# Kernel optimization log

Hardware: AMD Instinct MI355X
Metric: run time of the kernel (lower is better)

The kernel has to match this reference:

```python
import jax, jax.numpy as jnp
import numpy as np

N = 20000
D = 256      # input_dim
F = 256      # output_dim
K = F // 8   # hypernetwork rank (c=8 in source)


def setup_inputs() -> dict:
    key = jax.random.key(0)
    k1, k2, k3, k4, k5 = jax.random.split(key, 5)
    h = jax.random.normal(k1, (N, D), dtype=jnp.float32)
    adj = jax.random.uniform(k2, (N, N), dtype=jnp.float32)
    # xavier-uniform-like small init for params
    W1 = jax.random.normal(k3, (D, K), dtype=jnp.float32) * 0.05
    W2 = jax.random.normal(k4, (K, D, F), dtype=jnp.float32) * 0.05
    b = jax.random.normal(k5, (K, F), dtype=jnp.float32) * 0.05
    return {"h": h, "adj": adj, "W1": W1, "W2": W2, "b": b}


def reference(h, adj, W1, W2, b):
    # node: per-node code vector [N, K]
    node = h @ W1
    # Original: w = einsum('nd,dcf->ncf', node, W2); x = einsum('nc,ncf->nf', h, w)
    # Algebraically identical but avoids the huge [N, D, F] intermediate by
    # contracting the input-dim axis first: [N,K,F] instead of [N,D,F].
    hw = jnp.einsum('nc,kcf->nkf', h, W2)      # [N, K, F]
    x = jnp.einsum('nk,nkf->nf', node, hw)     # [N, F]
    # graph aggregation
    x = adj @ x                                 # [N, F]
    # per-node bias generated from the node code
    x = x + node @ b                            # [N, F]
    return jax.nn.relu(x)
```

## Files before the change

kernel.cpp:

```cpp
#include <hip/hip_runtime.h>
#include <hip/hip_bf16.h>

#define Nn 20000
#define Dd 256
#define Ff 256
#define Kc 32

typedef __attribute__((ext_vector_type(8))) short short8;
typedef __attribute__((ext_vector_type(4))) short short4_t;
typedef __attribute__((ext_vector_type(4))) float float4_t;

static __device__ __forceinline__ short f2bf(float x) {
    union { float f; unsigned u; } v; v.f = x;
    unsigned r = v.u + 0x7FFFu + ((v.u >> 16) & 1u);
    return (short)(r >> 16);
}
static __device__ __forceinline__ short4_t cvt4(float4_t v) {
    short4_t r; r[0] = f2bf(v[0]); r[1] = f2bf(v[1]); r[2] = f2bf(v[2]); r[3] = f2bf(v[3]);
    return r;
}

__global__ __launch_bounds__(256) void k_node(const float* __restrict__ h,
                                              const float* __restrict__ W1,
                                              float* __restrict__ node) {
    int t = blockIdx.x * 256 + threadIdx.x;
    int n = t >> 5, k = t & 31;
    if (n >= Nn) return;
    const float4_t* hr = (const float4_t*)(h + (size_t)n * Dd);
    float s = 0.f;
    #pragma unroll 8
    for (int d4 = 0; d4 < 64; ++d4) {
        float4_t hv = hr[d4];
        #pragma unroll
        for (int j = 0; j < 4; ++j) s += hv[j] * W1[(d4 * 4 + j) * Kc + k];
    }
    node[n * Kc + k] = s;
}

__global__ __launch_bounds__(256) void k_packW2(const float* __restrict__ W2,
                                                short* __restrict__ P) {
    int t = blockIdx.x * 256 + threadIdx.x;
    int lane = t & 63;
    int cf = (t >> 6) & 15;
    int dc = (t >> 10) & 7;
    int kk = t >> 13;
    int col = cf * 16 + (lane & 15);
    int d0  = dc * 32 + (lane >> 4) * 8;
    const float* src = W2 + ((size_t)(kk * Dd + d0)) * Ff + col;
    short8 v;
    #pragma unroll
    for (int j = 0; j < 8; ++j) v[j] = f2bf(src[(size_t)j * Ff]);
    *(short8*)(P + (size_t)t * 8) = v;
}

__global__ __launch_bounds__(256, 2) void k_xpre(const float* __restrict__ h,
                                                 const float* __restrict__ node,
                                                 const short* __restrict__ P,
                                                 short* __restrict__ xpre_t) {
    __shared__ short hlds[64 * 264];
    __shared__ float ntl[32 * 64];
    int t = threadIdx.x;
    int n0 = blockIdx.x * 64;

    #pragma unroll
    for (int i = 0; i < 16; ++i) {
        int c = t + i * 256;
        int row = c >> 6, cc = c & 63;
        int n = n0 + row; if (n > Nn - 1) n = Nn - 1;
        float4_t v = *(const float4_t*)(h + (size_t)n * Dd + cc * 4);
        *(short4_t*)&hlds[row * 264 + cc * 4] = cvt4(v);
    }
    #pragma unroll
    for (int i = 0; i < 8; ++i) {
        int idx = t + i * 256;
        int nl = idx >> 5, k = idx & 31;
        int n = n0 + nl; if (n > Nn - 1) n = Nn - 1;
        ntl[k * 64 + nl] = node[(size_t)n * Kc + k];
    }
    __syncthreads();

    int lane = t & 63, w = t >> 6;
    int arow = lane & 15;
    int asel = (lane >> 4) * 8;
    float4_t acc[4][4];
    #pragma unroll
    for (int a = 0; a < 4; ++a)
        #pragma unroll
        for (int b2 = 0; b2 < 4; ++b2) acc[a][b2] = (float4_t){0.f, 0.f, 0.f, 0.f};

    for (int kk = 0; kk < 32; ++kk) {
        float4_t T[4][4];
        #pragma unroll
        for (int a = 0; a < 4; ++a)
            #pragma unroll
            for (int b2 = 0; b2 < 4; ++b2) T[a][b2] = (float4_t){0.f, 0.f, 0.f, 0.f};
        #pragma unroll
        for (int dc = 0; dc < 8; ++dc) {
            short8 af[4], bfr[4];
            #pragma unroll
            for (int rf = 0; rf < 4; ++rf)
                af[rf] = *(const short8*)&hlds[(rf * 16 + arow) * 264 + dc * 32 + asel];
            #pragma unroll
            for (int cf = 0; cf < 4; ++cf)
                bfr[cf] = *(const short8*)(P + ((size_t)(((kk * 8 + dc) * 16 + w * 4 + cf) * 64 + lane)) * 8);
            #pragma unroll
            for (int rf = 0; rf < 4; ++rf)
                #pragma unroll
                for (int cf = 0; cf < 4; ++cf)
                    T[rf][cf] = __builtin_amdgcn_mfma_f32_16x16x32_bf16(af[rf], bfr[cf], T[rf][cf], 0, 0, 0);
        }
        #pragma unroll
        for (int rf = 0; rf < 4; ++rf) {
            float4_t sc = *(const float4_t*)&ntl[kk * 64 + rf * 16 + (lane >> 4) * 4];
            #pragma unroll
            for (int cf = 0; cf < 4; ++cf)
                #pragma unroll
                for (int r = 0; r < 4; ++r)
                    acc[rf][cf][r] += sc[r] * T[rf][cf][r];
        }
    }

    #pragma unroll
    for (int rf = 0; rf < 4; ++rf) {
        int nl = rf * 16 + (lane >> 4) * 4;
        #pragma unroll
        for (int cf = 0; cf < 4; ++cf) {
            int f = w * 64 + cf * 16 + (lane & 15);
            #pragma unroll
            for (int r = 0; r < 4; ++r) {
                int n = n0 + nl + r;
                if (n < Nn) xpre_t[(size_t)f * Nn + n] = f2bf(acc[rf][cf][r]);
            }
        }
    }
}

#define BM 80
#define BK 160
#define ASTR 168
#define NSTEP 125

__global__ __launch_bounds__(512, 2) void k_aggr(const float* __restrict__ adj,
                                                 const short* __restrict__ xpre_t,
                                                 const float* __restrict__ node,
                                                 const float* __restrict__ bb,
                                                 float* __restrict__ out) {
    __shared__ short alds[2][BM * ASTR];
    __shared__ float nlds[BM * 32];
    __shared__ float blds[32 * 256];

    const int t = threadIdx.x;
    const int m0 = blockIdx.x * BM;
    const int lane = t & 63, w = t >> 6;
    const int kb = (lane >> 4) * 8;

    #pragma unroll
    for (int i = 0; i < 5; ++i) { int idx = t + i * 512; nlds[idx] = node[(size_t)m0 * 32 + idx]; }
    #pragma unroll
    for (int i = 0; i < 4; ++i) { int idx = t + i * 512; *(float4_t*)&blds[idx * 4] = *(const float4_t*)(bb + (size_t)idx * 4); }

    const bool val7 = (t < 128);
    long gbase[7]; int loff[7];
    #pragma unroll
    for (int i = 0; i < 7; ++i) {
        int c = t + i * 512; if (c >= 3200) c = 0;
        int row = c / 40, col = c % 40;
        gbase[i] = (long)(m0 + row) * Nn + col * 4;
        loff[i]  = row * ASTR + col * 4;
    }
    const long xb0 = (long)(w * 32 + (lane & 15)) * Nn + kb;
    const long xb1 = xb0 + 16L * Nn;

#define LOADA(dst, s_) do { _Pragma("unroll") for (int i = 0; i < 7; ++i) \
        if (i < 6 || val7) dst[i] = *(const float4_t*)(adj + gbase[i] + (long)(s_) * BK); } while (0)

#define WRITEA(src, buf_) do { _Pragma("unroll") for (int i = 0; i < 7; ++i) \
        if (i < 6 || val7) *(short4_t*)&alds[buf_][loff[i]] = cvt4(src[i]); } while (0)

#define LOADB(d0_, d1_, s_) do { _Pragma("unroll") for (int dc = 0; dc < 5; ++dc) { \
        d0_[dc] = *(const short8*)(xpre_t + xb0 + (long)(s_) * BK + dc * 32); \
        d1_[dc] = *(const short8*)(xpre_t + xb1 + (long)(s_) * BK + dc * 32); } } while (0)

#define COMPUTE(buf_, B0_, B1_) do { _Pragma("unroll") for (int dc = 0; dc < 5; ++dc) { \
        _Pragma("unroll") for (int rf = 0; rf < 5; ++rf) { \
            short8 afr = *(const short8*)&alds[buf_][(rf * 16 + (lane & 15)) * ASTR + dc * 32 + kb]; \
            acc[rf][0] = __builtin_amdgcn_mfma_f32_16x16x32_bf16(afr, B0_[dc], acc[rf][0], 0, 0, 0); \
            acc[rf][1] = __builtin_amdgcn_mfma_f32_16x16x32_bf16(afr, B1_[dc], acc[rf][1], 0, 0, 0); } } } while (0)

#define SYNC() do { asm volatile("s_waitcnt lgkmcnt(0)" ::: "memory"); \
                    __builtin_amdgcn_s_barrier(); } while (0)

    float4_t acc[5][2];
    #pragma unroll
    for (int rf = 0; rf < 5; ++rf)
        #pragma unroll
        for (int cf = 0; cf < 2; ++cf) acc[rf][cf] = (float4_t){0.f, 0.f, 0.f, 0.f};

    float4_t A0[7], A1[7];
    short8 BA0[5], BA1[5], BB0[5], BB1[5];

    LOADA(A0, 0);
    LOADA(A1, 1);
    LOADB(BA0, BA1, 0);
    LOADB(BB0, BB1, 1);
    WRITEA(A0, 0);
    SYNC();

    #pragma unroll 1
    for (int p = 0; p < 62; ++p) {
        const int s0 = 2 * p;
        LOADA(A0, s0 + 2);
        COMPUTE(0, BA0, BA1);
        LOADB(BA0, BA1, s0 + 2);
        WRITEA(A1, 1);
        SYNC();
        if (s0 + 3 < NSTEP) LOADA(A1, s0 + 3);
        COMPUTE(1, BB0, BB1);
        if (s0 + 3 < NSTEP) LOADB(BB0, BB1, s0 + 3);
        WRITEA(A0, 0);
        SYNC();
    }
    COMPUTE(0, BA0, BA1);

    #pragma unroll
    for (int rf = 0; rf < 5; ++rf) {
        #pragma unroll
        for (int cf = 0; cf < 2; ++cf) {
            int fl = w * 32 + cf * 16 + (lane & 15);
            #pragma unroll
            for (int r = 0; r < 4; ++r) {
                int nl = rf * 16 + (lane >> 4) * 4 + r;
                float bias = 0.f;
                #pragma unroll 8
                for (int k = 0; k < 32; ++k) bias += nlds[nl * 32 + k] * blds[k * 256 + fl];
                float v = acc[rf][cf][r] + bias;
                out[(size_t)(m0 + nl) * 256 + fl] = v > 0.f ? v : 0.f;
            }
        }
    }
#undef LOADA
#undef WRITEA
#undef LOADB
#undef COMPUTE
#undef SYNC
}

extern "C" void kernel_launch(void* const* d_in, const int* in_sizes, int n_in,
                              void* d_out, int out_size, void* d_ws, size_t ws_size,
                              hipStream_t stream) {
    const float* h   = (const float*)d_in[0];
    const float* adj = (const float*)d_in[1];
    const float* W1  = (const float*)d_in[2];
    const float* W2  = (const float*)d_in[3];
    const float* b   = (const float*)d_in[4];
    float* out = (float*)d_out;

    char* ws = (char*)d_ws;
    float* node   = (float*)ws;
    short* P      = (short*)(ws + 2560000);
    short* xpre_t = (short*)(ws + 2560000 + 4194304);

    k_node  <<<2500, 256, 0, stream>>>(h, W1, node);
    k_packW2<<<1024, 256, 0, stream>>>(W2, P);
    k_xpre  <<<313,  256, 0, stream>>>(h, node, P, xpre_t);
    k_aggr  <<<250,  512, 0, stream>>>(adj, xpre_t, node, b, out);
}
```

Measured before the change: 868.3 us.

## Double BK to 320, pad xpre_t, restructure aggregation pipeline single-stage

Doubles the K-tile of the adj@x aggregation to 320 columns, which gives 63 steps with one barrier each. The single-step pipeline prefetches the next adj tile into registers while the MFMAs run, replacing the earlier two-stage register double-buffering. xpre_t is padded to 20160 columns and zero-filled so the last partial tile reads zeros, and adj reads are clamped to stay in bounds. The fp32 to bf16 conversion now uses the packed v_cvt_pk_bf16_f32 instruction. The changes aim to cut barrier and loop overhead, but they use more LDS and registers per block, which may lower occupancy under the 2-blocks-per-SM launch bound.

```diff
diff --git a/kernel.cpp b/kernel.cpp
--- a/kernel.cpp
+++ b/kernel.cpp
@@ -2,6 +2,7 @@
 #include <hip/hip_bf16.h>
 
 #define Nn 20000
+#define Npad 20160
 #define Dd 256
 #define Ff 256
 #define Kc 32
@@ -9,6 +10,7 @@
 typedef __attribute__((ext_vector_type(8))) short short8;
 typedef __attribute__((ext_vector_type(4))) short short4_t;
 typedef __attribute__((ext_vector_type(4))) float float4_t;
+typedef __attribute__((ext_vector_type(2))) unsigned int uint2_t;
 
 static __device__ __forceinline__ short f2bf(float x) {
     union { float f; unsigned u; } v; v.f = x;
@@ -17,6 +19,11 @@
 }
 static __device__ __forceinline__ short4_t cvt4(float4_t v) {
     short4_t r; r[0] = f2bf(v[0]); r[1] = f2bf(v[1]); r[2] = f2bf(v[2]); r[3] = f2bf(v[3]);
+    return r;
+}
+static __device__ __forceinline__ unsigned cvtpk(float a, float b) {
+    unsigned r;
+    asm("v_cvt_pk_bf16_f32 %0, %1, %2" : "=v"(r) : "v"(a), "v"(b));
     return r;
 }
 
@@ -129,16 +136,19 @@
             #pragma unroll
             for (int r = 0; r < 4; ++r) {
                 int n = n0 + nl + r;
-                if (n < Nn) xpre_t[(size_t)f * Nn + n] = f2bf(acc[rf][cf][r]);
+                if (n < Nn)       xpre_t[(size_t)f * Npad + n] = f2bf(acc[rf][cf][r]);
+                else if (n < Npad) xpre_t[(size_t)f * Npad + n] = 0;
             }
         }
     }
 }
 
 #define BM 80
-#define BK 160
-#define ASTR 168
-#define NSTEP 125
+#define BK 320
+#define DCN 10
+#define ASTR 328
+#define NSTEP 63
+#define ALIM (Nn * Nn - 4)
 
 __global__ __launch_bounds__(512, 2) void k_aggr(const float* __restrict__ adj,
                                                  const short* __restrict__ xpre_t,
@@ -159,68 +169,68 @@
     #pragma unroll
     for (int i = 0; i < 4; ++i) { int idx = t + i * 512; *(float4_t*)&blds[idx * 4] = *(const float4_t*)(bb + (size_t)idx * 4); }
 
-    const bool val7 = (t < 128);
-    long gbase[7]; int loff[7];
-    #pragma unroll
-    for (int i = 0; i < 7; ++i) {
-        int c = t + i * 512; if (c >= 3200) c = 0;
-        int row = c / 40, col = c % 40;
-        gbase[i] = (long)(m0 + row) * Nn + col * 4;
+    const bool v13 = (t < 256);
+    int gbase[13], loff[13];
+    #pragma unroll
+    for (int i = 0; i < 13; ++i) {
+        int c = t + i * 512; if (c >= 6400) c = 0;
+        int row = c / 80, col = c % 80;
+        gbase[i] = (m0 + row) * Nn + col * 4;
         loff[i]  = row * ASTR + col * 4;
     }
-    const long xb0 = (long)(w * 32 + (lane & 15)) * Nn + kb;
-    const long xb1 = xb0 + 16L * Nn;
-
-#define LOADA(dst, s_) do { _Pragma("unroll") for (int i = 0; i < 7; ++i) \
-        if (i < 6 || val7) dst[i] = *(const float4_t*)(adj + gbase[i] + (long)(s_) * BK); } while (0)
-
-#define WRITEA(src, buf_) do { _Pragma("unroll") for (int i = 0; i < 7; ++i) \
-        if (i < 6 || val7) *(short4_t*)&alds[buf_][loff[i]] = cvt4(src[i]); } while (0)
-
-#define LOADB(d0_, d1_, s_) do { _Pragma("unroll") for (int dc = 0; dc < 5; ++dc) { \
-        d0_[dc] = *(const short8*)(xpre_t + xb0 + (long)(s_) * BK + dc * 32); \
-        d1_[dc] = *(const short8*)(xpre_t + xb1 + (long)(s_) * BK + dc * 32); } } while (0)
-
-#define COMPUTE(buf_, B0_, B1_) do { _Pragma("unroll") for (int dc = 0; dc < 5; ++dc) { \
-        _Pragma("unroll") for (int rf = 0; rf < 5; ++rf) { \
-            short8 afr = *(const short8*)&alds[buf_][(rf * 16 + (lane & 15)) * ASTR + dc * 32 + kb]; \
-            acc[rf][0] = __builtin_amdgcn_mfma_f32_16x16x32_bf16(afr, B0_[dc], acc[rf][0], 0, 0, 0); \
-            acc[rf][1] = __builtin_amdgcn_mfma_f32_16x16x32_bf16(afr, B1_[dc], acc[rf][1], 0, 0, 0); } } } while (0)
+    const short* xrow0 = xpre_t + (long)(w * 32 + (lane & 15)) * Npad + kb;
+    const short* xrow1 = xrow0 + 16L * Npad;
+
+    float4_t acc[5][2];
+    #pragma unroll
+    for (int rf = 0; rf < 5; ++rf)
+        #pragma unroll
+        for (int cf = 0; cf < 2; ++cf) acc[rf][cf] = (float4_t){0.f, 0.f, 0.f, 0.f};
+
+    float4_t A[13];
+    short8 b0[DCN], b1[DCN];
+
+#define LOADA(s_) do { _Pragma("unroll") for (int i = 0; i < 13; ++i) \
+        if (i < 12 || v13) { int idx = gbase[i] + (s_) * BK; \
+            if (idx > ALIM) idx = ALIM; \
+            A[i] = *(const float4_t*)(adj + idx); } } while (0)
+
+#define WRITEA(buf_) do { _Pragma("unroll") for (int i = 0; i < 13; ++i) \
+        if (i < 12 || v13) { \
+            uint2_t u = { cvtpk(A[i][0], A[i][1]), cvtpk(A[i][2], A[i][3]) }; \
+            *(uint2_t*)&alds[buf_][loff[i]] = u; } } while (0)
 
 #define SYNC() do { asm volatile("s_waitcnt lgkmcnt(0)" ::: "memory"); \
                     __builtin_amdgcn_s_barrier(); } while (0)
 
-    float4_t acc[5][2];
-    #pragma unroll
-    for (int rf = 0; rf < 5; ++rf)
-        #pragma unroll
-        for (int cf = 0; cf < 2; ++cf) acc[rf][cf] = (float4_t){0.f, 0.f, 0.f, 0.f};
-
-    float4_t A0[7], A1[7];
-    short8 BA0[5], BA1[5], BB0[5], BB1[5];
-
-    LOADA(A0, 0);
-    LOADA(A1, 1);
-    LOADB(BA0, BA1, 0);
-    LOADB(BB0, BB1, 1);
-    WRITEA(A0, 0);
+    LOADA(0);
+    WRITEA(0);
     SYNC();
 
     #pragma unroll 1
-    for (int p = 0; p < 62; ++p) {
-        const int s0 = 2 * p;
-        LOADA(A0, s0 + 2);
-        COMPUTE(0, BA0, BA1);
-        LOADB(BA0, BA1, s0 + 2);
-        WRITEA(A1, 1);
+    for (int s = 0; s < NSTEP; ++s) {
+        const short* xr0 = xrow0 + (long)s * BK;
+        const short* xr1 = xrow1 + (long)s * BK;
+        #pragma unroll
+        for (int dc = 0; dc < DCN; ++dc) {
+            b0[dc] = *(const short8*)(xr0 + dc * 32);
+            b1[dc] = *(const short8*)(xr1 + dc * 32);
+        }
+        if (s + 1 < NSTEP) LOADA(s + 1);
+
+        const short* ar = alds[s & 1];
+        #pragma unroll
+        for (int dc = 0; dc < DCN; ++dc) {
+            #pragma unroll
+            for (int rf = 0; rf < 5; ++rf) {
+                short8 afr = *(const short8*)&ar[(rf * 16 + (lane & 15)) * ASTR + dc * 32 + kb];
+                acc[rf][0] = __builtin_amdgcn_mfma_f32_16x16x32_bf16(afr, b0[dc], acc[rf][0], 0, 0, 0);
+                acc[rf][1] = __builtin_amdgcn_mfma_f32_16x16x32_bf16(afr, b1[dc], acc[rf][1], 0, 0, 0);
+            }
+        }
+        if (s + 1 < NSTEP) WRITEA((s & 1) ^ 1);
         SYNC();
-        if (s0 + 3 < NSTEP) LOADA(A1, s0 + 3);
-        COMPUTE(1, BB0, BB1);
-        if (s0 + 3 < NSTEP) LOADB(BB0, BB1, s0 + 3);
-        WRITEA(A0, 0);
-        SYNC();
-    }
-    COMPUTE(0, BA0, BA1);
+    }
 
     #pragma unroll
     for (int rf = 0; rf < 5; ++rf) {
@@ -240,8 +250,6 @@
     }
 #undef LOADA
 #undef WRITEA
-#undef LOADB
-#undef COMPUTE
 #undef SYNC
 }
 
@@ -262,6 +270,6 @@
 
     k_node  <<<2500, 256, 0, stream>>>(h, W1, node);
     k_packW2<<<1024, 256, 0, stream>>>(W2, P);
-    k_xpre  <<<313,  256, 0, stream>>>(h, node, P, xpre_t);
+    k_xpre  <<<315,  256, 0, stream>>>(h, node, P, xpre_t);
     k_aggr  <<<250,  512, 0, stream>>>(adj, xpre_t, node, b, out);
 }
```

After: 924.8 us. 1.07x slower.
